# Kernel optimization log

Hardware: AMD Instinct MI355X
Metric: run time of the kernel (lower is better)

## Reference

```python
import jax, jax.numpy as jnp
import numpy as np

EPS = 1e-08

def setup_inputs() -> dict:
    key = jax.random.key(0)
    k1, k2, k3, k4 = jax.random.split(key, 4)
    B, N, IN, OUT, WF = 16, 4096, 512, 512, 512
    x = jax.random.normal(k1, (B, N, IN), dtype=jnp.float32)
    w = jax.random.normal(k2, (B, WF), dtype=jnp.float32)
    # kaiming-normal-like init for the main weight
    weight = jax.random.normal(k3, (OUT, IN), dtype=jnp.float32) * np.sqrt(2.0 / IN)
    bias = jnp.zeros((OUT,), dtype=jnp.float32)
    A_w = jax.random.normal(k4, (IN, WF), dtype=jnp.float32) * np.sqrt(1.0 / WF)
    A_b = jnp.zeros((IN,), dtype=jnp.float32)
    return {"x": x, "w": w, "weight": weight, "bias": bias, "A_w": A_w, "A_b": A_b}

def reference(x, w, weight, bias, A_w, A_b):
    # style -> per-input-channel scale: (B, in)
    s = w @ A_w.T + A_b
    # modulate: (B, out, in)
    wm = weight[None, :, :] * s[:, None, :]
    # demodulate: rsqrt over in-dim
    norm = jax.lax.rsqrt(EPS + jnp.sum(wm * wm, axis=2, keepdims=True))
    wd = wm * norm
    # batched matmul: (B, N, in) x (B, out, in) -> (B, N, out)
    out = jnp.einsum('bni,boi->bno', x, wd) + bias
    return jax.nn.relu(out)
```

## Files before the change

### kernel.cpp

```cpp
#include <hip/hip_runtime.h>
#include <hip/hip_bf16.h>

#define B_    16
#define M_    4096
#define K_    512
#define O_    512

#define BM 128
#define BN 128
#define BK 32

typedef float f32x4 __attribute__((ext_vector_type(4)));
typedef short bf16x8 __attribute__((ext_vector_type(8)));

__device__ __forceinline__ unsigned short f2bf(float f) {
    unsigned int u = __builtin_bit_cast(unsigned int, f);
    u += 0x7fffu + ((u >> 16) & 1u);
    return (unsigned short)(u >> 16);
}

__global__ void style_kernel(const float* __restrict__ w, const float* __restrict__ A_w,
                             const float* __restrict__ A_b, float* __restrict__ s) {
    int b = blockIdx.x;
    int i = blockIdx.y * 64 + threadIdx.x;
    __shared__ float wsh[512];
    for (int j = threadIdx.x; j < 512; j += 64) wsh[j] = w[b * 512 + j];
    __syncthreads();
    const float* arow = A_w + (size_t)i * 512;
    float acc = 0.f;
    #pragma unroll 4
    for (int f = 0; f < 512; f += 4) {
        float4 a = *(const float4*)(arow + f);
        acc += a.x * wsh[f] + a.y * wsh[f + 1] + a.z * wsh[f + 2] + a.w * wsh[f + 3];
    }
    s[b * 512 + i] = acc + A_b[i];
}

__global__ void demod_kernel(const float* __restrict__ weight, const float* __restrict__ s,
                             unsigned short* __restrict__ wd) {
    int gw = blockIdx.x * 4 + (threadIdx.x >> 6);
    int lane = threadIdx.x & 63;
    int b = gw >> 9;
    int o = gw & 511;
    const float* wrow = weight + (size_t)o * 512;
    const float* srow = s + b * 512;
    float vals[8];
    float ss = 0.f;
    #pragma unroll
    for (int j = 0; j < 8; j++) {
        int i = lane + j * 64;
        float v = wrow[i] * srow[i];
        vals[j] = v;
        ss += v * v;
    }
    #pragma unroll
    for (int off = 32; off; off >>= 1) ss += __shfl_xor(ss, off);
    float nrm = rsqrtf(1e-8f + ss);
    unsigned short* drow = wd + ((size_t)b * 512 + o) * 512;
    #pragma unroll
    for (int j = 0; j < 8; j++) {
        int i = lane + j * 64;
        drow[i] = f2bf(vals[j] * nrm);
    }
}

__global__ __launch_bounds__(256) void gemm_kernel(const float* __restrict__ x,
                                                   const unsigned short* __restrict__ wd,
                                                   const float* __restrict__ bias,
                                                   float* __restrict__ out) {
    __shared__ unsigned short sA[BM * BK];
    __shared__ unsigned short sB[BN * BK];

    const int b  = blockIdx.z;
    const int m0 = blockIdx.y * BM;
    const int n0 = blockIdx.x * BN;
    const float* xb = x + (size_t)b * M_ * K_;
    const unsigned short* wdb = wd + (size_t)b * O_ * K_;

    const int t = threadIdx.x;
    const int w = t >> 6;
    const int l = t & 63;
    const int wave_row = (w >> 1) * 64;
    const int wave_col = (w & 1) * 64;
    const int lrow  = l & 15;
    const int khalf = (l >> 4) * 8;

    f32x4 acc[4][4] = {};

    for (int kk = 0; kk < K_; kk += BK) {
        #pragma unroll
        for (int j = 0; j < 4; j++) {
            int e = (j * 256 + t) * 4;
            int r = e >> 5, c = e & 31;
            float4 v = *(const float4*)(xb + (m0 + r) * K_ + kk + c);
            union { __hip_bfloat162 h2[2]; unsigned long long u64; } cv;
            cv.h2[0] = __float22bfloat162_rn(float2{v.x, v.y});
            cv.h2[1] = __float22bfloat162_rn(float2{v.z, v.w});
            *(unsigned long long*)(&sA[e]) = cv.u64;
        }
        #pragma unroll
        for (int j = 0; j < 2; j++) {
            int e = (j * 256 + t) * 8;
            int r = e >> 5, c = e & 31;
            __builtin_amdgcn_global_load_lds(
                (const __attribute__((address_space(1))) unsigned int*)(wdb + (n0 + r) * K_ + kk + c),
                (__attribute__((address_space(3))) unsigned int*)(&sB[e]),
                16, 0, 0);
        }
        __syncthreads();

        bf16x8 af[4], bfr[4];
        #pragma unroll
        for (int mi = 0; mi < 4; mi++)
            af[mi] = *(const bf16x8*)(&sA[(wave_row + mi * 16 + lrow) * BK + khalf]);
        #pragma unroll
        for (int ni = 0; ni < 4; ni++)
            bfr[ni] = *(const bf16x8*)(&sB[(wave_col + ni * 16 + lrow) * BK + khalf]);
        #pragma unroll
        for (int mi = 0; mi < 4; mi++)
            #pragma unroll
            for (int ni = 0; ni < 4; ni++)
                acc[mi][ni] = __builtin_amdgcn_mfma_f32_16x16x32_bf16(af[mi], bfr[ni], acc[mi][ni], 0, 0, 0);
        __syncthreads();
    }

    const int col_l = l & 15;
    const int row_q = (l >> 4) * 4;
    #pragma unroll
    for (int ni = 0; ni < 4; ni++) {
        int o = n0 + wave_col + ni * 16 + col_l;
        float bv = bias[o];
        #pragma unroll
        for (int mi = 0; mi < 4; mi++) {
            int mrow = m0 + wave_row + mi * 16 + row_q;
            #pragma unroll
            for (int r = 0; r < 4; r++) {
                float v = acc[mi][ni][r] + bv;
                out[((size_t)b * M_ + mrow + r) * O_ + o] = v > 0.f ? v : 0.f;
            }
        }
    }
}

extern "C" void kernel_launch(void* const* d_in, const int* in_sizes, int n_in,
                              void* d_out, int out_size, void* d_ws, size_t ws_size,
                              hipStream_t stream) {
    const float* x      = (const float*)d_in[0];
    const float* w      = (const float*)d_in[1];
    const float* weight = (const float*)d_in[2];
    const float* bias   = (const float*)d_in[3];
    const float* A_w    = (const float*)d_in[4];
    const float* A_b    = (const float*)d_in[5];
    float* out = (float*)d_out;

    unsigned short* wd = (unsigned short*)d_ws;
    float* s = (float*)((char*)d_ws + (size_t)B_ * O_ * K_ * sizeof(unsigned short));

    style_kernel<<<dim3(B_, 8), 64, 0, stream>>>(w, A_w, A_b, s);
    demod_kernel<<<(B_ * O_) / 4, 256, 0, stream>>>(weight, s, wd);
    gemm_kernel<<<dim3(O_ / BN, M_ / BM, B_), 256, 0, stream>>>(x, wd, bias, out);
}
```

Measured before the change: 308.7 us.

## Double-buffer GEMM tiles with register prefetch, swizzled LDS, and XCD-aware block mapping

Rewrites the GEMM main loop to double-buffer the A and B tiles in LDS. The next x tile is prefetched into registers and the next weight tile is loaded via global_load_lds while MFMAs run on the current buffer, leaving one barrier per iteration instead of two. LDS chunks are XOR-swizzled to reduce bank conflicts on the fragment reads. A 1D grid is remapped so that blocks on the same XCD share m-rows and batch, which should improve L2 reuse of x. Launch bounds request 3 blocks per CU, which could constrain registers and cause spills.

```diff
diff --git a/kernel.cpp b/kernel.cpp
--- a/kernel.cpp
+++ b/kernel.cpp
@@ -12,11 +12,10 @@
 
 typedef float f32x4 __attribute__((ext_vector_type(4)));
 typedef short bf16x8 __attribute__((ext_vector_type(8)));
-
-__device__ __forceinline__ unsigned short f2bf(float f) {
-    unsigned int u = __builtin_bit_cast(unsigned int, f);
-    u += 0x7fffu + ((u >> 16) & 1u);
-    return (unsigned short)(u >> 16);
+typedef unsigned short u16x8 __attribute__((ext_vector_type(8)));
+
+__device__ __forceinline__ int chunk_off(int row, int kq) {
+    return (row * 4 + (kq ^ ((row >> 1) & 3))) * 8;
 }
 
 __global__ void style_kernel(const float* __restrict__ w, const float* __restrict__ A_w,
@@ -60,20 +59,28 @@
     #pragma unroll
     for (int j = 0; j < 8; j++) {
         int i = lane + j * 64;
-        drow[i] = f2bf(vals[j] * nrm);
-    }
-}
-
-__global__ __launch_bounds__(256) void gemm_kernel(const float* __restrict__ x,
-                                                   const unsigned short* __restrict__ wd,
-                                                   const float* __restrict__ bias,
-                                                   float* __restrict__ out) {
-    __shared__ unsigned short sA[BM * BK];
-    __shared__ unsigned short sB[BN * BK];
-
-    const int b  = blockIdx.z;
-    const int m0 = blockIdx.y * BM;
-    const int n0 = blockIdx.x * BN;
+        unsigned int u = __builtin_bit_cast(unsigned int, vals[j] * nrm);
+        u += 0x7fffu + ((u >> 16) & 1u);
+        drow[i] = (unsigned short)(u >> 16);
+    }
+}
+
+__global__ __launch_bounds__(256, 3) void gemm_kernel(const float* __restrict__ x,
+                                                      const unsigned short* __restrict__ wd,
+                                                      const float* __restrict__ bias,
+                                                      float* __restrict__ out) {
+    __shared__ unsigned short sA[2][BM * BK];
+    __shared__ unsigned short sB[2][BN * BK];
+
+    int g = blockIdx.x;
+    int xcd = g & 7;
+    int grp = g >> 3;
+    int nblk = grp & 3;
+    int mb = xcd * 64 + (grp >> 2);
+    const int b  = mb >> 5;
+    const int m0 = (mb & 31) * BM;
+    const int n0 = nblk * BN;
+
     const float* xb = x + (size_t)b * M_ * K_;
     const unsigned short* wdb = wd + (size_t)b * O_ * K_;
 
@@ -83,45 +90,93 @@
     const int wave_row = (w >> 1) * 64;
     const int wave_col = (w & 1) * 64;
     const int lrow  = l & 15;
-    const int khalf = (l >> 4) * 8;
+    const int kq_l  = l >> 4;
+
+    int offA[4], offB[4];
+    #pragma unroll
+    for (int mi = 0; mi < 4; mi++)
+        offA[mi] = chunk_off(wave_row + mi * 16 + lrow, kq_l);
+    #pragma unroll
+    for (int ni = 0; ni < 4; ni++)
+        offB[ni] = chunk_off(wave_col + ni * 16 + lrow, kq_l);
+
+    const int ar = t >> 1;
+    const int akq0 = (t & 1) * 2;
+    const float* abase = xb + (size_t)(m0 + ar) * K_ + akq0 * 8;
+
+    int bchunk[2], brow[2], bkq[2];
+    #pragma unroll
+    for (int j = 0; j < 2; j++) {
+        int c = w * 128 + j * 64 + l;
+        brow[j] = c >> 2;
+        bkq[j] = (c & 3) ^ ((brow[j] >> 1) & 3);
+        bchunk[j] = c;
+    }
 
     f32x4 acc[4][4] = {};
-
+    f32x4 areg[4];
+
+    #pragma unroll
+    for (int j = 0; j < 2; j++) {
+        __builtin_amdgcn_global_load_lds(
+            (const __attribute__((address_space(1))) unsigned int*)(wdb + (size_t)(n0 + brow[j]) * K_ + bkq[j] * 8),
+            (__attribute__((address_space(3))) unsigned int*)(&sB[0][bchunk[j] * 8]),
+            16, 0, 0);
+    }
+    #pragma unroll
+    for (int j = 0; j < 4; j++) areg[j] = *(const f32x4*)(abase + j * 4);
+    #pragma unroll
+    for (int j = 0; j < 2; j++) {
+        union { __hip_bfloat162 h[4]; u16x8 v; } cv;
+        cv.h[0] = __float22bfloat162_rn(float2{areg[2*j][0], areg[2*j][1]});
+        cv.h[1] = __float22bfloat162_rn(float2{areg[2*j][2], areg[2*j][3]});
+        cv.h[2] = __float22bfloat162_rn(float2{areg[2*j+1][0], areg[2*j+1][1]});
+        cv.h[3] = __float22bfloat162_rn(float2{areg[2*j+1][2], areg[2*j+1][3]});
+        *(u16x8*)(&sA[0][chunk_off(ar, akq0 + j)]) = cv.v;
+    }
+    __syncthreads();
+
+    int cur = 0;
+    #pragma unroll 2
     for (int kk = 0; kk < K_; kk += BK) {
-        #pragma unroll
-        for (int j = 0; j < 4; j++) {
-            int e = (j * 256 + t) * 4;
-            int r = e >> 5, c = e & 31;
-            float4 v = *(const float4*)(xb + (m0 + r) * K_ + kk + c);
-            union { __hip_bfloat162 h2[2]; unsigned long long u64; } cv;
-            cv.h2[0] = __float22bfloat162_rn(float2{v.x, v.y});
-            cv.h2[1] = __float22bfloat162_rn(float2{v.z, v.w});
-            *(unsigned long long*)(&sA[e]) = cv.u64;
+        int nxt = cur ^ 1;
+        bool pf = (kk + BK) < K_;
+        if (pf) {
+            #pragma unroll
+            for (int j = 0; j < 2; j++) {
+                __builtin_amdgcn_global_load_lds(
+                    (const __attribute__((address_space(1))) unsigned int*)(wdb + (size_t)(n0 + brow[j]) * K_ + kk + BK + bkq[j] * 8),
+                    (__attribute__((address_space(3))) unsigned int*)(&sB[nxt][bchunk[j] * 8]),
+                    16, 0, 0);
+            }
+            #pragma unroll
+            for (int j = 0; j < 4; j++) areg[j] = *(const f32x4*)(abase + kk + BK + j * 4);
         }
-        #pragma unroll
-        for (int j = 0; j < 2; j++) {
-            int e = (j * 256 + t) * 8;
-            int r = e >> 5, c = e & 31;
-            __builtin_amdgcn_global_load_lds(
-                (const __attribute__((address_space(1))) unsigned int*)(wdb + (n0 + r) * K_ + kk + c),
-                (__attribute__((address_space(3))) unsigned int*)(&sB[e]),
-                16, 0, 0);
+
+        bf16x8 af[4], bfr[4];
+        #pragma unroll
+        for (int mi = 0; mi < 4; mi++) af[mi] = *(const bf16x8*)(&sA[cur][offA[mi]]);
+        #pragma unroll
+        for (int ni = 0; ni < 4; ni++) bfr[ni] = *(const bf16x8*)(&sB[cur][offB[ni]]);
+        #pragma unroll
+        for (int mi = 0; mi < 4; mi++)
+            #pragma unroll
+            for (int ni = 0; ni < 4; ni++)
+                acc[mi][ni] = __builtin_amdgcn_mfma_f32_16x16x32_bf16(af[mi], bfr[ni], acc[mi][ni], 0, 0, 0);
+
+        if (pf) {
+            #pragma unroll
+            for (int j = 0; j < 2; j++) {
+                union { __hip_bfloat162 h[4]; u16x8 v; } cv;
+                cv.h[0] = __float22bfloat162_rn(float2{areg[2*j][0], areg[2*j][1]});
+                cv.h[1] = __float22bfloat162_rn(float2{areg[2*j][2], areg[2*j][3]});
+                cv.h[2] = __float22bfloat162_rn(float2{areg[2*j+1][0], areg[2*j+1][1]});
+                cv.h[3] = __float22bfloat162_rn(float2{areg[2*j+1][2], areg[2*j+1][3]});
+                *(u16x8*)(&sA[nxt][chunk_off(ar, akq0 + j)]) = cv.v;
+            }
         }
         __syncthreads();
-
-        bf16x8 af[4], bfr[4];
-        #pragma unroll
-        for (int mi = 0; mi < 4; mi++)
-            af[mi] = *(const bf16x8*)(&sA[(wave_row + mi * 16 + lrow) * BK + khalf]);
-        #pragma unroll
-        for (int ni = 0; ni < 4; ni++)
-            bfr[ni] = *(const bf16x8*)(&sB[(wave_col + ni * 16 + lrow) * BK + khalf]);
-        #pragma unroll
-        for (int mi = 0; mi < 4; mi++)
-            #pragma unroll
-            for (int ni = 0; ni < 4; ni++)
-                acc[mi][ni] = __builtin_amdgcn_mfma_f32_16x16x32_bf16(af[mi], bfr[ni], acc[mi][ni], 0, 0, 0);
-        __syncthreads();
+        cur = nxt;
     }
 
     const int col_l = l & 15;
@@ -158,5 +213,5 @@
 
     style_kernel<<<dim3(B_, 8), 64, 0, stream>>>(w, A_w, A_b, s);
     demod_kernel<<<(B_ * O_) / 4, 256, 0, stream>>>(weight, s, wd);
-    gemm_kernel<<<dim3(O_ / BN, M_ / BM, B_), 256, 0, stream>>>(x, wd, bias, out);
-}
+    gemm_kernel<<<2048, 256, 0, stream>>>(x, wd, bias, out);
+}
```

Result: no change. 306.7 us (-0.6%).

## Fold style scale into x and apply demod norm in GEMM epilogue

Applied to the files above, without the earlier changes.

Instead of materializing a per-batch demodulated bf16 weight tensor, the weight is cast to bf16 once and shared across batches. The style scale is multiplied into x during the bf16 conversion, and the per-output norm is applied in the epilogue. The GEMM also gains double-buffered LDS with register prefetch (one sync per k-step), an XOR-swizzled LDS layout, an XCD-aware block remap, and launch bounds for 4 waves. The intent is to remove the large wd write/read and improve latency hiding. The cost is extra register pressure and a different rounding order from scaling x instead of the weight.

```diff
diff --git a/kernel.cpp b/kernel.cpp
--- a/kernel.cpp
+++ b/kernel.cpp
@@ -12,11 +12,10 @@
 
 typedef float f32x4 __attribute__((ext_vector_type(4)));
 typedef short bf16x8 __attribute__((ext_vector_type(8)));
-
-__device__ __forceinline__ unsigned short f2bf(float f) {
-    unsigned int u = __builtin_bit_cast(unsigned int, f);
-    u += 0x7fffu + ((u >> 16) & 1u);
-    return (unsigned short)(u >> 16);
+typedef unsigned short u16x8 __attribute__((ext_vector_type(8)));
+
+__device__ __forceinline__ int chunk_off(int row, int kq) {
+    return (row * 4 + (kq ^ ((row >> 1) & 3))) * 8;
 }
 
 __global__ void style_kernel(const float* __restrict__ w, const float* __restrict__ A_w,
@@ -36,46 +35,55 @@
     s[b * 512 + i] = acc + A_b[i];
 }
 
-__global__ void demod_kernel(const float* __restrict__ weight, const float* __restrict__ s,
-                             unsigned short* __restrict__ wd) {
+__global__ void nrm_kernel(const float* __restrict__ weight, const float* __restrict__ s,
+                           float* __restrict__ nrm) {
     int gw = blockIdx.x * 4 + (threadIdx.x >> 6);
     int lane = threadIdx.x & 63;
     int b = gw >> 9;
     int o = gw & 511;
     const float* wrow = weight + (size_t)o * 512;
     const float* srow = s + b * 512;
-    float vals[8];
     float ss = 0.f;
     #pragma unroll
     for (int j = 0; j < 8; j++) {
         int i = lane + j * 64;
         float v = wrow[i] * srow[i];
-        vals[j] = v;
         ss += v * v;
     }
     #pragma unroll
     for (int off = 32; off; off >>= 1) ss += __shfl_xor(ss, off);
-    float nrm = rsqrtf(1e-8f + ss);
-    unsigned short* drow = wd + ((size_t)b * 512 + o) * 512;
-    #pragma unroll
-    for (int j = 0; j < 8; j++) {
-        int i = lane + j * 64;
-        drow[i] = f2bf(vals[j] * nrm);
-    }
-}
-
-__global__ __launch_bounds__(256) void gemm_kernel(const float* __restrict__ x,
-                                                   const unsigned short* __restrict__ wd,
-                                                   const float* __restrict__ bias,
-                                                   float* __restrict__ out) {
-    __shared__ unsigned short sA[BM * BK];
-    __shared__ unsigned short sB[BN * BK];
-
-    const int b  = blockIdx.z;
-    const int m0 = blockIdx.y * BM;
-    const int n0 = blockIdx.x * BN;
+    if (lane == 0) nrm[b * 512 + o] = rsqrtf(1e-8f + ss);
+}
+
+__global__ void wcast_kernel(const float* __restrict__ weight, unsigned short* __restrict__ wb) {
+    int e = (blockIdx.x * 256 + threadIdx.x) * 4;
+    float4 v = *(const float4*)(weight + e);
+    union { __hip_bfloat162 h[2]; unsigned long long u; } cv;
+    cv.h[0] = __float22bfloat162_rn(float2{v.x, v.y});
+    cv.h[1] = __float22bfloat162_rn(float2{v.z, v.w});
+    *(unsigned long long*)(wb + e) = cv.u;
+}
+
+__global__ __launch_bounds__(256, 4) void gemm_kernel(const float* __restrict__ x,
+                                                      const unsigned short* __restrict__ wb,
+                                                      const float* __restrict__ s,
+                                                      const float* __restrict__ nrm,
+                                                      const float* __restrict__ bias,
+                                                      float* __restrict__ out) {
+    __shared__ unsigned short sA[2][BM * BK];
+    __shared__ unsigned short sB[2][BN * BK];
+    __shared__ float sS[K_];
+
+    int g = blockIdx.x;
+    int xcd = g & 7;
+    int grp = g >> 3;
+    int nblk = grp & 3;
+    int mb = xcd * 64 + (grp >> 2);
+    const int b  = mb >> 5;
+    const int m0 = (mb & 31) * BM;
+    const int n0 = nblk * BN;
+
     const float* xb = x + (size_t)b * M_ * K_;
-    const unsigned short* wdb = wd + (size_t)b * O_ * K_;
 
     const int t = threadIdx.x;
     const int w = t >> 6;
@@ -83,45 +91,73 @@
     const int wave_row = (w >> 1) * 64;
     const int wave_col = (w & 1) * 64;
     const int lrow  = l & 15;
-    const int khalf = (l >> 4) * 8;
+    const int kq_l  = l >> 4;
+
+    *(float2*)(&sS[t * 2]) = *(const float2*)(s + b * K_ + t * 2);
+
+    int offA[4], offB[4];
+    #pragma unroll
+    for (int mi = 0; mi < 4; mi++) offA[mi] = chunk_off(wave_row + mi * 16 + lrow, kq_l);
+    #pragma unroll
+    for (int ni = 0; ni < 4; ni++) offB[ni] = chunk_off(wave_col + ni * 16 + lrow, kq_l);
+
+    const int ar = t >> 1;
+    const int aq = t & 1;
+    const float* abase = xb + (size_t)(m0 + ar) * K_ + aq * 16;
+    const unsigned short* bbase = wb + (size_t)(n0 + ar) * K_ + aq * 16;
+
+    f32x4 araw[4];
+    u16x8 braw[2];
+    #pragma unroll
+    for (int j = 0; j < 4; j++) araw[j] = *(const f32x4*)(abase + j * 4);
+    #pragma unroll
+    for (int j = 0; j < 2; j++) braw[j] = *(const u16x8*)(bbase + j * 8);
+
+    __syncthreads();
 
     f32x4 acc[4][4] = {};
 
-    for (int kk = 0; kk < K_; kk += BK) {
-        #pragma unroll
-        for (int j = 0; j < 4; j++) {
-            int e = (j * 256 + t) * 4;
-            int r = e >> 5, c = e & 31;
-            float4 v = *(const float4*)(xb + (m0 + r) * K_ + kk + c);
-            union { __hip_bfloat162 h2[2]; unsigned long long u64; } cv;
-            cv.h2[0] = __float22bfloat162_rn(float2{v.x, v.y});
-            cv.h2[1] = __float22bfloat162_rn(float2{v.z, v.w});
-            *(unsigned long long*)(&sA[e]) = cv.u64;
+    #pragma unroll 2
+    for (int i = 0; i < 16; i++) {
+        const int kk = i * BK;
+        const int buf = i & 1;
+
+        #pragma unroll
+        for (int j = 0; j < 2; j++) {
+            f32x4 s0 = *(const f32x4*)(&sS[kk + aq * 16 + j * 8]);
+            f32x4 s1 = *(const f32x4*)(&sS[kk + aq * 16 + j * 8 + 4]);
+            f32x4 p0 = araw[2 * j] * s0;
+            f32x4 p1 = araw[2 * j + 1] * s1;
+            union { __hip_bfloat162 h[4]; u16x8 v; } cv;
+            cv.h[0] = __float22bfloat162_rn(float2{p0[0], p0[1]});
+            cv.h[1] = __float22bfloat162_rn(float2{p0[2], p0[3]});
+            cv.h[2] = __float22bfloat162_rn(float2{p1[0], p1[1]});
+            cv.h[3] = __float22bfloat162_rn(float2{p1[2], p1[3]});
+            *(u16x8*)(&sA[buf][chunk_off(ar, aq * 2 + j)]) = cv.v;
         }
         #pragma unroll
-        for (int j = 0; j < 2; j++) {
-            int e = (j * 256 + t) * 8;
-            int r = e >> 5, c = e & 31;
-            __builtin_amdgcn_global_load_lds(
-                (const __attribute__((address_space(1))) unsigned int*)(wdb + (n0 + r) * K_ + kk + c),
-                (__attribute__((address_space(3))) unsigned int*)(&sB[e]),
-                16, 0, 0);
+        for (int j = 0; j < 2; j++)
+            *(u16x8*)(&sB[buf][chunk_off(ar, aq * 2 + j)]) = braw[j];
+
+        if (i < 15) {
+            #pragma unroll
+            for (int j = 0; j < 4; j++) araw[j] = *(const f32x4*)(abase + kk + BK + j * 4);
+            #pragma unroll
+            for (int j = 0; j < 2; j++) braw[j] = *(const u16x8*)(bbase + kk + BK + j * 8);
         }
+
         __syncthreads();
 
         bf16x8 af[4], bfr[4];
         #pragma unroll
-        for (int mi = 0; mi < 4; mi++)
-            af[mi] = *(const bf16x8*)(&sA[(wave_row + mi * 16 + lrow) * BK + khalf]);
-        #pragma unroll
-        for (int ni = 0; ni < 4; ni++)
-            bfr[ni] = *(const bf16x8*)(&sB[(wave_col + ni * 16 + lrow) * BK + khalf]);
+        for (int mi = 0; mi < 4; mi++) af[mi] = *(const bf16x8*)(&sA[buf][offA[mi]]);
+        #pragma unroll
+        for (int ni = 0; ni < 4; ni++) bfr[ni] = *(const bf16x8*)(&sB[buf][offB[ni]]);
         #pragma unroll
         for (int mi = 0; mi < 4; mi++)
             #pragma unroll
             for (int ni = 0; ni < 4; ni++)
                 acc[mi][ni] = __builtin_amdgcn_mfma_f32_16x16x32_bf16(af[mi], bfr[ni], acc[mi][ni], 0, 0, 0);
-        __syncthreads();
     }
 
     const int col_l = l & 15;
@@ -130,12 +166,13 @@
     for (int ni = 0; ni < 4; ni++) {
         int o = n0 + wave_col + ni * 16 + col_l;
         float bv = bias[o];
+        float nv = nrm[b * 512 + o];
         #pragma unroll
         for (int mi = 0; mi < 4; mi++) {
             int mrow = m0 + wave_row + mi * 16 + row_q;
             #pragma unroll
             for (int r = 0; r < 4; r++) {
-                float v = acc[mi][ni][r] + bv;
+                float v = acc[mi][ni][r] * nv + bv;
                 out[((size_t)b * M_ + mrow + r) * O_ + o] = v > 0.f ? v : 0.f;
             }
         }
@@ -153,10 +190,12 @@
     const float* A_b    = (const float*)d_in[5];
     float* out = (float*)d_out;
 
-    unsigned short* wd = (unsigned short*)d_ws;
-    float* s = (float*)((char*)d_ws + (size_t)B_ * O_ * K_ * sizeof(unsigned short));
+    unsigned short* wbf = (unsigned short*)d_ws;
+    float* s   = (float*)((char*)d_ws + 512 * 1024);
+    float* nrm = (float*)((char*)d_ws + 512 * 1024 + 32 * 1024);
 
     style_kernel<<<dim3(B_, 8), 64, 0, stream>>>(w, A_w, A_b, s);
-    demod_kernel<<<(B_ * O_) / 4, 256, 0, stream>>>(weight, s, wd);
-    gemm_kernel<<<dim3(O_ / BN, M_ / BM, B_), 256, 0, stream>>>(x, wd, bias, out);
-}
+    wcast_kernel<<<(O_ * K_) / 1024, 256, 0, stream>>>(weight, wbf);
+    nrm_kernel<<<(B_ * O_) / 4, 256, 0, stream>>>(weight, s, nrm);
+    gemm_kernel<<<2048, 256, 0, stream>>>(x, wbf, s, nrm, bias, out);
+}
```

New measurement: 315.4 us. +2.2%, slower.
